# Kernel optimization log

Hardware: AMD Instinct MI355X
Metric: run time of the kernel (lower is better)

The kernel has to match this reference:

```python
import jax, jax.numpy as jnp
import numpy as np
from jax import lax

# MinkowskiEngine semantics reproduced on a dense grid:
# - a sparse tensor's active set = voxels where any feature channel is nonzero
# - stride-1 conv: output coords == input coords  -> mask output with input mask
# - stride-2 conv (k=5, pad=2): output coords = unique(floor(c/2))  -> 2x2x2 max-pool of mask
# - GlobalPooling: mean of features over active output coords, per batch
# MinkowskiConvolution has no bias by default; MinkowskiLinear has one.

DN = ('NCDHW', 'OIDHW', 'NCDHW')

def conv3d(x, w, stride, pad):
    return lax.conv_general_dilated(
        x, w, (stride, stride, stride), [(pad, pad)] * 3, dimension_numbers=DN)

def pool_mask(m):
    # occupancy of stride-2 output coords: any active voxel in each 2x2x2 block
    B, T, H, W = m.shape
    return m.reshape(B, T // 2, 2, H // 2, 2, W // 2, 2).max(axis=(2, 4, 6))

def setup_inputs() -> dict:
    key = jax.random.key(0)
    ks = jax.random.split(key, 7)
    B, T, C, H, W = 16, 128, 2, 34, 34
    vals = jax.random.normal(ks[0], (B, T, C, H, W), jnp.float32)
    keep = jax.random.bernoulli(ks[1], 0.05, (B, T, 1, H, W)).astype(jnp.float32)
    x = vals * keep
    w1 = jax.random.normal(ks[2], (32, 2, 5, 5, 5), jnp.float32) * 0.05
    w2 = jax.random.normal(ks[3], (64, 32, 5, 5, 5), jnp.float32) * 0.05
    w3 = jax.random.normal(ks[4], (128, 64, 3, 3, 3), jnp.float32) * 0.05
    wl = jax.random.normal(ks[5], (10, 128), jnp.float32) * 0.05
    bl = jnp.zeros((10,), jnp.float32)
    return {"x": x, "w1": w1, "w2": w2, "w3": w3, "wl": wl, "bl": bl}

def reference(x, w1, w2, w3, wl, bl):
    # x: [B, T, C, H, W] -> permute(0,2,1,3,4) -> [B, C, T, H, W]
    dense = jnp.transpose(x, (0, 2, 1, 3, 4))
    # active coordinate set of ME.to_sparse(dense)
    mask = (jnp.abs(dense).sum(axis=1) > 0).astype(dense.dtype)  # [B, T, H, W]
    mask = lax.stop_gradient(mask)
    m1 = mask[:, None]
    h = conv3d(dense, w1, 1, 2) * m1                         # k5 s1, out coords = in coords
    mask2 = pool_mask(mask)                                  # stride-2 output occupancy
    m2 = mask2[:, None]
    h = jax.nn.relu(conv3d(h, w2, 2, 2)) * m2                # k5 s2 + ReLU
    h = jax.nn.relu(conv3d(h, w3, 1, 1)) * m2                # k3 s1 + ReLU
    cnt = jnp.maximum(mask2.sum(axis=(1, 2, 3)), 1.0)[:, None]
    pooled = h.sum(axis=(2, 3, 4)) / cnt                     # global avg over active coords -> [B,128]
    logits = pooled @ wl.T + bl                              # MinkowskiLinear(128,10)
    return jax.nn.softmax(jax.nn.relu(logits), axis=-1)      # ReLU -> Softmax -> ToFeature [B,10]
```

## Files before the change

### kernel.cpp

```cpp
#include <hip/hip_runtime.h>

#define BB 16
#define TT 128
#define HH 34
#define WW 34
#define HWSZ (HH*WW)
#define NP1 (BB*TT*HH*WW)
#define TD 64
#define HD 17
#define WD 17
#define NP2 (BB*TD*HD*WD)
#define NW1 (NP1/64)
#define NW2 (NP2/64)
#define CAP1 262144
#define CAP2 131072
#define G2 1024
#define G3 768

typedef __attribute__((ext_vector_type(8))) short bf16x8;
typedef __attribute__((ext_vector_type(4))) float f32x4;

__device__ inline unsigned short f2bf(float f) {
  unsigned u = __float_as_uint(f);
  unsigned r = (u + 0x7fff + ((u >> 16) & 1)) >> 16;
  return (unsigned short)r;
}
__device__ inline float bf2f(unsigned short s) {
  return __uint_as_float((unsigned)s << 16);
}

__global__ void k_ballot1(const float* __restrict__ x, unsigned long long* __restrict__ b1) {
  int i = blockIdx.x * 256 + threadIdx.x;
  int hw = i % HWSZ;
  int bt = i / HWSZ;
  const float* px = x + (size_t)bt * 2 * HWSZ + hw;
  bool act = (fabsf(px[0]) + fabsf(px[HWSZ])) > 0.0f;
  unsigned long long m = __ballot(act);
  if ((threadIdx.x & 63) == 0) b1[i >> 6] = m;
}

__global__ void k_ballot2(const unsigned long long* __restrict__ b1,
                          unsigned long long* __restrict__ b2) {
  int i = blockIdx.x * 256 + threadIdx.x;
  if (i >= NP2) return;
  int ow = i % WD; int r = i / WD;
  int oh = r % HD; r /= HD;
  int od = r % TD; int b = r / TD;
  bool act = false;
  for (int dt = 0; dt < 2; dt++)
    for (int dh = 0; dh < 2; dh++)
      for (int dw = 0; dw < 2; dw++) {
        int t = od * 2 + dt, h = oh * 2 + dh, w = ow * 2 + dw;
        int lin = ((b * TT + t) * HH + h) * WW + w;
        if ((b1[lin >> 6] >> (lin & 63)) & 1ull) act = true;
      }
  unsigned long long m = __ballot(act);
  if ((threadIdx.x & 63) == 0) b2[i >> 6] = m;
}

__global__ __launch_bounds__(1024) void k_scan(
    const unsigned long long* __restrict__ b1, const unsigned long long* __restrict__ b2,
    int* __restrict__ wb1, int* __restrict__ wb2,
    int* __restrict__ counter1, int* __restrict__ counter2, float* __restrict__ cnt) {
  __shared__ int wsum[16];
  __shared__ int wpre[16];
  __shared__ int tots[2];
  int tid = threadIdx.x, lane = tid & 63, wv = tid >> 6;

  const int CH1 = (NW1 + 1023) / 1024;
  int lo = tid * CH1, hi = min(lo + CH1, NW1);
  int s = 0;
  for (int i = lo; i < hi; i++) s += __popcll(b1[i]);
  int sc = s;
  #pragma unroll
  for (int d = 1; d < 64; d <<= 1) { int y = __shfl_up(sc, d); if (lane >= d) sc += y; }
  if (lane == 63) wsum[wv] = sc;
  __syncthreads();
  if (wv == 0 && lane < 16) {
    int v = wsum[lane];
    int p = v;
    #pragma unroll
    for (int d = 1; d < 16; d <<= 1) { int y = __shfl_up(p, d); if (lane >= d) p += y; }
    wpre[lane] = p - v;
    if (lane == 15) tots[0] = p;
  }
  __syncthreads();
  {
    int base = wpre[wv] + (sc - s);
    for (int i = lo; i < hi; i++) { wb1[i] = base; base += __popcll(b1[i]); }
  }
  if (tid == 0) *counter1 = tots[0];
  __syncthreads();

  const int CH2 = (NW2 + 1023) / 1024;
  lo = tid * CH2; hi = min(lo + CH2, NW2);
  s = 0;
  for (int i = lo; i < hi; i++) s += __popcll(b2[i]);
  sc = s;
  #pragma unroll
  for (int d = 1; d < 64; d <<= 1) { int y = __shfl_up(sc, d); if (lane >= d) sc += y; }
  if (lane == 63) wsum[wv] = sc;
  __syncthreads();
  if (wv == 0 && lane < 16) {
    int v = wsum[lane];
    int p = v;
    #pragma unroll
    for (int d = 1; d < 16; d <<= 1) { int y = __shfl_up(p, d); if (lane >= d) p += y; }
    wpre[lane] = p - v;
    if (lane == 15) tots[1] = p;
  }
  __syncthreads();
  {
    int base = wpre[wv] + (sc - s);
    for (int i = lo; i < hi; i++) { wb2[i] = base; base += __popcll(b2[i]); }
  }
  if (tid == 0) *counter2 = tots[1];
  __syncthreads();
  if (tid < 16) {
    int c0 = wb2[tid * 289];
    int c1 = (tid == 15) ? tots[1] : wb2[(tid + 1) * 289];
    cnt[tid] = (float)(c1 - c0);
  }
}

__global__ void k_fill1(const unsigned long long* __restrict__ b1,
                        const int* __restrict__ wb1, int* __restrict__ idx1) {
  int i = blockIdx.x * 256 + threadIdx.x;
  unsigned long long m = b1[i >> 6];
  int lane = i & 63;
  int p = -1;
  if ((m >> lane) & 1ull) {
    p = wb1[i >> 6] + __popcll(m & ((1ull << lane) - 1ull));
    if (p >= CAP1) p = -1;
  }
  idx1[i] = p;
}

__global__ void k_fill2(const unsigned long long* __restrict__ b2,
                        const int* __restrict__ wb2,
                        int* __restrict__ idx2, int* __restrict__ list2) {
  int i = blockIdx.x * 256 + threadIdx.x;
  if (i >= NP2) return;
  unsigned long long m = b2[i >> 6];
  int lane = i & 63;
  int p = -1;
  if ((m >> lane) & 1ull) {
    p = wb2[i >> 6] + __popcll(m & ((1ull << lane) - 1ull));
    if (p < CAP2) list2[p] = i; else p = -1;
  }
  idx2[i] = p;
}

__global__ __launch_bounds__(256) void k_conv1e(
    const float* __restrict__ x, const float* __restrict__ w1,
    const unsigned long long* __restrict__ b1, const int* __restrict__ wb1,
    unsigned short* __restrict__ h1c) {
  __shared__ unsigned short w1s[8000];
  __shared__ unsigned int plist[384];
  __shared__ unsigned long long q[4][128];
  __shared__ int pcnt;
  int tid = threadIdx.x;
  int b = blockIdx.x >> 7;
  int t0 = blockIdx.x & 127;
  if (tid == 0) pcnt = 0;
  for (int j = tid; j < 8000; j += 256) w1s[j] = f2bf(w1[j]);
  __syncthreads();
  int slabbase = (b * TT + t0) * HWSZ;
  for (int hw = tid; hw < HWSZ; hw += 256) {
    int lin = slabbase + hw;
    unsigned long long m = b1[lin >> 6];
    int ln = lin & 63;
    if ((m >> ln) & 1ull) {
      int p = wb1[lin >> 6] + __popcll(m & ((1ull << ln) - 1ull));
      if (p < CAP1) {
        int s = atomicAdd(&pcnt, 1);
        if (s < 384) plist[s] = ((unsigned)p << 11) | (unsigned)hw;
      }
    }
  }
  __syncthreads();
  int n = min(pcnt, 384);
  int lane = tid & 63, wid = tid >> 6;
  int oc = lane & 31, c = lane >> 5;
  int woff = (oc * 2 + c) * 125;
  int csh = c * 16;
  int kt = lane / 5, kh = lane - kt * 5;
  const float* xb = x + (size_t)b * TT * 2 * HWSZ;
  for (int li = wid; li < n; li += 4) {
    unsigned e = plist[li];
    int hw = e & 0x7ff;
    int p = e >> 11;
    int h_ = hw / 34, w_ = hw - h_ * 34;
    int cntA = 0;
    unsigned m5 = 0;
    int t2 = 0, h2 = 0;
    if (lane < 25) {
      t2 = t0 + kt - 2;
      h2 = h_ + kh - 2;
      if ((unsigned)t2 < TT && (unsigned)h2 < HH) {
        int kwmin = (w_ < 2) ? (2 - w_) : 0;
        int kwmax = (w_ > 31) ? (35 - w_) : 4;
        int lin = ((b * TT + t2) * HH + h2) * WW + (w_ + kwmin - 2);
        int wi = lin >> 6, sh = lin & 63;
        unsigned long long v = b1[wi] >> sh;
        if (sh > 59) v |= b1[wi + 1] << (64 - sh);
        m5 = ((unsigned)v & ((1u << (kwmax - kwmin + 1)) - 1u)) << kwmin;
        cntA = __popc(m5);
      }
    }
    int inc = cntA;
    #pragma unroll
    for (int d = 1; d < 64; d <<= 1) { int y = __shfl_up(inc, d); if (lane >= d) inc += y; }
    int off = inc - cntA;
    int ne = __shfl(inc, 63);
    unsigned mm = m5;
    while (mm) {
      int kw = __ffs(mm) - 1; mm &= mm - 1;
      int w2 = w_ + kw - 2;
      int xoff = (t2 * 2) * HWSZ + h2 * 34 + w2;
      unsigned short xv0 = f2bf(xb[xoff]);
      unsigned short xv1 = f2bf(xb[xoff + HWSZ]);
      int tap = (kt * 5 + kh) * 5 + kw;
      q[wid][off++] = (unsigned long long)((unsigned)xv0 | ((unsigned)xv1 << 16)) |
                      ((unsigned long long)tap << 32);
    }
    float acc = 0.f;
    for (int e2 = 0; e2 < ne; e2++) {
      unsigned long long ent = q[wid][e2];
      int tap = (int)(ent >> 32);
      float xv = bf2f((unsigned short)((ent >> csh) & 0xffffull));
      acc += xv * bf2f(w1s[woff + tap]);
    }
    float other = __shfl_down(acc, 32);
    if (lane < 32) h1c[(size_t)p * 32 + oc] = f2bf(acc + other);
  }
}

__global__ void k_tw2b(const float* __restrict__ w2, unsigned short* __restrict__ w2b) {
  int i = blockIdx.x * blockDim.x + threadIdx.x;
  if (i >= 125 * 64 * 32) return;
  int c = i & 31; int r = i >> 5;
  int oc = r & 63; int tap = r >> 6;
  w2b[i] = f2bf(w2[((size_t)oc * 32 + c) * 125 + tap]);
}
__global__ void k_tw3b(const float* __restrict__ w3, unsigned short* __restrict__ w3b) {
  int i = blockIdx.x * blockDim.x + threadIdx.x;
  if (i >= 27 * 128 * 64) return;
  int c = i & 63; int r = i >> 6;
  int oc = r & 127; int tap = r >> 7;
  w3b[i] = f2bf(w3[((size_t)oc * 64 + c) * 27 + tap]);
}

#define S2 40
#define M2 128
__global__ __launch_bounds__(256) void k_conv2m(
    const unsigned short* __restrict__ h1c,
    const unsigned short* __restrict__ w2b,
    const int* __restrict__ idx1,
    const int* __restrict__ list2, const int* __restrict__ counter2,
    unsigned short* __restrict__ h2c) {
  __shared__ __align__(16) unsigned short As[2][M2 * S2];
  __shared__ __align__(16) unsigned short Bs[2][64 * S2];
  __shared__ int4 mc[M2];
  __shared__ int klut[125];
  int tid = threadIdx.x;
  int lane = tid & 63, wid = tid >> 6;
  int fr = lane & 15, fq = lane >> 4;
  int wr = wid * 32;
  if (tid < 125) {
    int kt = tid / 25, r2 = tid - kt * 25;
    klut[tid] = kt | ((r2 / 5) << 4) | ((r2 % 5) << 8);
  }
  int count2 = min(*counter2, CAP2);
  int nchunk = (count2 + M2 - 1) >> 7;
  int aspos = tid >> 1, asq = tid & 1;
  int bspos = tid >> 2, bsq = tid & 3;
  int chid = (blockIdx.x & 7) * (G2 >> 3) + (blockIdx.x >> 3);
  __syncthreads();
  for (int ch = chid; ch < nchunk; ch += gridDim.x) {
    __syncthreads();
    if (tid < M2) {
      int p = ch * M2 + tid;
      int m = (p < count2) ? list2[p] : -1;
      int4 qq; qq.x = -1; qq.y = 0; qq.z = 0; qq.w = 0;
      if (m >= 0) {
        int ow = m % WD; int r = m / WD;
        int oh = r % HD; r /= HD;
        qq.x = r / TD; qq.y = r % TD; qq.z = oh; qq.w = ow;
      }
      mc[tid] = qq;
    }
    __syncthreads();
    int4 q = mc[aspos];
    int tb = q.y * 2 - 2, hb = q.z * 2 - 2, wbv = q.w * 2 - 2;
    bool bok = q.x >= 0;
    auto rowfor = [&](int tap) -> int {
      int k = klut[tap];
      int t = tb + (k & 15), h = hb + ((k >> 4) & 15), w = wbv + (k >> 8);
      int row = -1;
      if (bok && (unsigned)t < TT && (unsigned)h < HH && (unsigned)w < WW)
        row = idx1[((q.x * TT + t) * HH + h) * WW + w];
      return row;
    };
    f32x4 acc[2][4];
    #pragma unroll
    for (int i = 0; i < 2; i++)
      #pragma unroll
      for (int j = 0; j < 4; j++) acc[i][j] = (f32x4){0.f, 0.f, 0.f, 0.f};
    int rowN1;
    int4 rA0 = {0,0,0,0}, rA1 = {0,0,0,0}, rB;
    {
      int r0 = rowfor(0);
      if (r0 >= 0) {
        const unsigned short* s = h1c + (size_t)r0 * 32 + asq * 16;
        rA0 = *(const int4*)s;
        rA1 = *(const int4*)(s + 8);
      }
      rB = *(const int4*)(w2b + (size_t)bspos * 32 + bsq * 8);
      rowN1 = rowfor(1);
    }
    for (int tap = 0; tap < 125; ++tap) {
      int bsel = tap & 1;
      {
        unsigned short* ad = &As[bsel][aspos * S2 + asq * 16];
        *(int4*)(ad) = rA0;
        *(int4*)(ad + 8) = rA1;
        *(int4*)(&Bs[bsel][bspos * S2 + bsq * 8]) = rB;
      }
      bool more = tap < 124;
      if (more) {
        int4 v0 = {0,0,0,0}, v1 = {0,0,0,0};
        if (rowN1 >= 0) {
          const unsigned short* s = h1c + (size_t)rowN1 * 32 + asq * 16;
          v0 = *(const int4*)s;
          v1 = *(const int4*)(s + 8);
        }
        rA0 = v0; rA1 = v1;
        rB = *(const int4*)(w2b + (size_t)(tap + 1) * 2048 + bspos * 32 + bsq * 8);
        rowN1 = (tap < 123) ? rowfor(tap + 2) : -1;
      }
      __syncthreads();
      const unsigned short* ap = &As[bsel][(wr + fr) * S2 + fq * 8];
      const unsigned short* bp = &Bs[bsel][fr * S2 + fq * 8];
      bf16x8 a0 = *(const bf16x8*)ap;
      bf16x8 a1 = *(const bf16x8*)(ap + 16 * S2);
      #pragma unroll
      for (int ni = 0; ni < 4; ni++) {
        bf16x8 bfrag = *(const bf16x8*)(bp + ni * 16 * S2);
        acc[0][ni] = __builtin_amdgcn_mfma_f32_16x16x32_bf16(a0, bfrag, acc[0][ni], 0, 0, 0);
        acc[1][ni] = __builtin_amdgcn_mfma_f32_16x16x32_bf16(a1, bfrag, acc[1][ni], 0, 0, 0);
      }
    }
    int base = ch * M2;
    #pragma unroll
    for (int mi = 0; mi < 2; mi++)
      #pragma unroll
      for (int ni = 0; ni < 4; ni++)
        #pragma unroll
        for (int j = 0; j < 4; j++) {
          int r = wr + mi * 16 + fq * 4 + j;
          int p = base + r;
          if (p < count2) {
            int col = ni * 16 + fr;
            h2c[(size_t)p * 64 + col] = f2bf(fmaxf(acc[mi][ni][j], 0.f));
          }
        }
  }
}

#define S3 72
#define SH3 132
__global__ __launch_bounds__(256) void k_conv3m(
    const unsigned short* __restrict__ h2c,
    const unsigned short* __restrict__ w3b,
    const int* __restrict__ idx2,
    const int* __restrict__ list2, const int* __restrict__ counter2,
    float* __restrict__ partial) {
  __shared__ __align__(16) unsigned short As[2][64 * S3];
  __shared__ __align__(16) unsigned short Bs[2][128 * S3];
  __shared__ float pools[2048];
  __shared__ int rowsL[27 * 64];
  __shared__ int4 mc[64];
  __shared__ int posb[64];
  int tid = threadIdx.x;
  int lane = tid & 63, wid = tid >> 6;
  int fr = lane & 15, fq = lane >> 4;
  int wr = (wid >> 1) * 32, wc = (wid & 1) * 64;
  for (int j = tid; j < 2048; j += 256) pools[j] = 0.f;
  int count2 = min(*counter2, CAP2);
  int nchunk = (count2 + 63) >> 6;
  int spos = tid >> 2, sq = tid & 3;
  int boc = tid >> 1, bh = tid & 1;
  int chid = (blockIdx.x & 7) * (G3 >> 3) + (blockIdx.x >> 3);
  for (int ch = chid; ch < nchunk; ch += gridDim.x) {
    __syncthreads();
    if (tid < 64) {
      int p = ch * 64 + tid;
      int m = (p < count2) ? list2[p] : -1;
      int4 q; q.x = -1; q.y = 0; q.z = 0; q.w = 0;
      if (m >= 0) {
        int ow = m % WD; int r = m / WD;
        int oh = r % HD; r /= HD;
        q.x = r / TD; q.y = r % TD; q.z = oh; q.w = ow;
      }
      mc[tid] = q;
      posb[tid] = (q.x >= 0) ? q.x : 0;
    }
    __syncthreads();
    for (int j = tid; j < 27 * 64; j += 256) {
      int tap = j >> 6, pos = j & 63;
      int4 q = mc[pos];
      int row = -1;
      if (q.x >= 0) {
        int dt = tap / 9 - 1, dh = (tap / 3) % 3 - 1, dw = tap % 3 - 1;
        int t = q.y + dt, h = q.z + dh, w = q.w + dw;
        if ((unsigned)t < TD && (unsigned)h < HD && (unsigned)w < WD)
          row = idx2[((q.x * TD + t) * HD + h) * WD + w];
      }
      rowsL[j] = row;
    }
    __syncthreads();
    f32x4 acc[2][4];
    #pragma unroll
    for (int i = 0; i < 2; i++)
      #pragma unroll
      for (int j = 0; j < 4; j++) acc[i][j] = (f32x4){0.f, 0.f, 0.f, 0.f};
    int4 rA0 = {0, 0, 0, 0}, rA1 = {0, 0, 0, 0};
    {
      int row = rowsL[spos];
      if (row >= 0) {
        const unsigned short* s = h2c + (size_t)row * 64 + sq * 16;
        rA0 = *(const int4*)s;
        rA1 = *(const int4*)(s + 8);
      }
    }
    int4 rB0, rB1, rB2, rB3;
    {
      const unsigned short* wsrc = w3b + (size_t)boc * 64 + bh * 32;
      rB0 = *(const int4*)(wsrc);
      rB1 = *(const int4*)(wsrc + 8);
      rB2 = *(const int4*)(wsrc + 16);
      rB3 = *(const int4*)(wsrc + 24);
    }
    for (int tap = 0; tap < 27; tap++) {
      int bsel = tap & 1;
      {
        unsigned short* ad = &As[bsel][spos * S3 + sq * 16];
        *(int4*)(ad) = rA0;
        *(int4*)(ad + 8) = rA1;
        unsigned short* bd = &Bs[bsel][boc * S3 + bh * 32];
        *(int4*)(bd) = rB0;
        *(int4*)(bd + 8) = rB1;
        *(int4*)(bd + 16) = rB2;
        *(int4*)(bd + 24) = rB3;
      }
      if (tap < 26) {
        int row = rowsL[(tap + 1) * 64 + spos];
        int4 v0 = {0, 0, 0, 0}, v1 = {0, 0, 0, 0};
        if (row >= 0) {
          const unsigned short* s = h2c + (size_t)row * 64 + sq * 16;
          v0 = *(const int4*)s;
          v1 = *(const int4*)(s + 8);
        }
        rA0 = v0; rA1 = v1;
        const unsigned short* wsrc = w3b + ((size_t)(tap + 1) * 128 + boc) * 64 + bh * 32;
        rB0 = *(const int4*)(wsrc);
        rB1 = *(const int4*)(wsrc + 8);
        rB2 = *(const int4*)(wsrc + 16);
        rB3 = *(const int4*)(wsrc + 24);
      }
      __syncthreads();
      const unsigned short* ap = &As[bsel][(wr + fr) * S3 + fq * 8];
      const unsigned short* bp = &Bs[bsel][(wc + fr) * S3 + fq * 8];
      #pragma unroll
      for (int kk = 0; kk < 2; kk++) {
        bf16x8 a0 = *(const bf16x8*)(ap + kk * 32);
        bf16x8 a1 = *(const bf16x8*)(ap + 16 * S3 + kk * 32);
        #pragma unroll
        for (int ni = 0; ni < 4; ni++) {
          bf16x8 bfrag = *(const bf16x8*)(bp + ni * 16 * S3 + kk * 32);
          acc[0][ni] = __builtin_amdgcn_mfma_f32_16x16x32_bf16(a0, bfrag, acc[0][ni], 0, 0, 0);
          acc[1][ni] = __builtin_amdgcn_mfma_f32_16x16x32_bf16(a1, bfrag, acc[1][ni], 0, 0, 0);
        }
      }
    }
    __syncthreads();
    unsigned short* h3 = &As[0][0];
    #pragma unroll
    for (int mi = 0; mi < 2; mi++)
      #pragma unroll
      for (int ni = 0; ni < 4; ni++)
        #pragma unroll
        for (int j = 0; j < 4; j++) {
          int r = wr + mi * 16 + fq * 4 + j;
          int col = wc + ni * 16 + fr;
          h3[r * SH3 + col] = f2bf(fmaxf(acc[mi][ni][j], 0.f));
        }
    __syncthreads();
    if (tid < 128) {
      for (int r = 0; r < 64; r++)
        pools[posb[r] * 128 + tid] += bf2f(h3[r * SH3 + tid]);
    }
  }
  __syncthreads();
  for (int j = tid; j < 2048; j += 256)
    partial[(size_t)blockIdx.x * 2048 + j] = pools[j];
}

__global__ __launch_bounds__(1024) void k_final(
    const float* __restrict__ partial, const float* __restrict__ cnt,
    const float* __restrict__ wl, const float* __restrict__ bl,
    float* __restrict__ out) {
  __shared__ float red[1024];
  __shared__ float pr[128];
  __shared__ float lg[10];
  int b = blockIdx.x;
  int tid = threadIdx.x;
  int c = tid & 127, sl = tid >> 7;
  float s = 0.f;
  for (int g = sl; g < G3; g += 8) s += partial[(size_t)g * 2048 + b * 128 + c];
  red[tid] = s;
  __syncthreads();
  if (tid < 128) {
    float t = 0.f;
    #pragma unroll
    for (int k = 0; k < 8; k++) t += red[k * 128 + tid];
    pr[tid] = t / fmaxf(cnt[b], 1.0f);
  }
  __syncthreads();
  if (tid < 10) {
    float acc = bl[tid];
    for (int j = 0; j < 128; j++) acc += pr[j] * wl[tid * 128 + j];
    lg[tid] = fmaxf(acc, 0.f);
  }
  __syncthreads();
  if (tid == 0) {
    float mx = lg[0];
    for (int k = 1; k < 10; k++) mx = fmaxf(mx, lg[k]);
    float se = 0.f;
    for (int k = 0; k < 10; k++) se += expf(lg[k] - mx);
    for (int k = 0; k < 10; k++) out[b * 10 + k] = expf(lg[k] - mx) / se;
  }
}

extern "C" void kernel_launch(void* const* d_in, const int* in_sizes, int n_in,
                              void* d_out, int out_size, void* d_ws, size_t ws_size,
                              hipStream_t stream) {
  const float* x  = (const float*)d_in[0];
  const float* w1 = (const float*)d_in[1];
  const float* w2 = (const float*)d_in[2];
  const float* w3 = (const float*)d_in[3];
  const float* wl = (const float*)d_in[4];
  const float* bl = (const float*)d_in[5];
  float* out = (float*)d_out;

  float* ws = (float*)d_ws;
  int* counter1 = (int*)(ws + 0);
  int* counter2 = (int*)(ws + 1);
  float* cnt = ws + 16;
  size_t off = 2080;
  unsigned long long* b1 = (unsigned long long*)(ws + off); off += NW1 * 2 + 2;
  unsigned long long* b2 = (unsigned long long*)(ws + off); off += NW2 * 2;
  int* wb1 = (int*)(ws + off); off += NW1;
  int* wb2 = (int*)(ws + off); off += NW2;
  int* idx1 = (int*)(ws + off); off += NP1;
  unsigned short* h1c = (unsigned short*)(ws + off); off += (size_t)CAP1 * 16;
  int* idx2 = (int*)(ws + off); off += NP2;
  int* list2 = (int*)(ws + off); off += CAP2;
  unsigned short* h2c = (unsigned short*)(ws + off); off += (size_t)CAP2 * 32;
  unsigned short* w2b = (unsigned short*)(ws + off); off += 128000;
  unsigned short* w3b = (unsigned short*)(ws + off); off += 110592;
  float* partial = ws + off; off += (size_t)G3 * 2048;

  hipMemsetAsync(d_ws, 0, 256, stream);

  k_tw2b<<<(256000 + 255) / 256, 256, 0, stream>>>(w2, w2b);
  k_tw3b<<<(221184 + 255) / 256, 256, 0, stream>>>(w3, w3b);
  k_ballot1<<<NP1 / 256, 256, 0, stream>>>(x, b1);
  k_ballot2<<<(NP2 + 255) / 256, 256, 0, stream>>>(b1, b2);
  k_scan<<<1, 1024, 0, stream>>>(b1, b2, wb1, wb2, counter1, counter2, cnt);
  k_conv1e<<<2048, 256, 0, stream>>>(x, w1, b1, wb1, h1c);
  k_fill1<<<NP1 / 256, 256, 0, stream>>>(b1, wb1, idx1);
  k_fill2<<<(NP2 + 255) / 256, 256, 0, stream>>>(b2, wb2, idx2, list2);
  k_conv2m<<<G2, 256, 0, stream>>>(h1c, w2b, idx1, list2, counter2, h2c);
  k_conv3m<<<G3, 256, 0, stream>>>(h2c, w3b, idx2, list2, counter2, partial);
  k_final<<<16, 1024, 0, stream>>>(partial, cnt, wl, bl, out);
}
```

Baseline: 413.4 us.

## Replace dense index maps with on-the-fly bitmap popcount lookups; split final reduction

Removes the dense idx1/idx2 index arrays and their fill kernels. conv2 and conv3 now compute a voxel's compact row from the occupancy bitmap word and the per-word prefix base with a popcount, which cuts a full-grid write pass and shrinks the gathered data. The final reduction is split into a wider 128-block reduce kernel plus a small head kernel, the conv3 grid shrinks, and LDS row strides are changed. The trade-off is extra ALU work and two dependent loads per neighbour lookup, and the new LDS padding may introduce bank conflicts.

Measured after the change: 1.039 ms. 151% more time.

```diff
diff --git a/kernel.cpp b/kernel.cpp
--- a/kernel.cpp
+++ b/kernel.cpp
@@ -15,7 +15,7 @@
 #define CAP1 262144
 #define CAP2 131072
 #define G2 1024
-#define G3 768
+#define G3 512
 
 typedef __attribute__((ext_vector_type(8))) short bf16x8;
 typedef __attribute__((ext_vector_type(4))) float f32x4;
@@ -123,32 +123,16 @@
   }
 }
 
-__global__ void k_fill1(const unsigned long long* __restrict__ b1,
-                        const int* __restrict__ wb1, int* __restrict__ idx1) {
-  int i = blockIdx.x * 256 + threadIdx.x;
-  unsigned long long m = b1[i >> 6];
-  int lane = i & 63;
-  int p = -1;
-  if ((m >> lane) & 1ull) {
-    p = wb1[i >> 6] + __popcll(m & ((1ull << lane) - 1ull));
-    if (p >= CAP1) p = -1;
-  }
-  idx1[i] = p;
-}
-
-__global__ void k_fill2(const unsigned long long* __restrict__ b2,
-                        const int* __restrict__ wb2,
-                        int* __restrict__ idx2, int* __restrict__ list2) {
+__global__ void k_list2(const unsigned long long* __restrict__ b2,
+                        const int* __restrict__ wb2, int* __restrict__ list2) {
   int i = blockIdx.x * 256 + threadIdx.x;
   if (i >= NP2) return;
   unsigned long long m = b2[i >> 6];
   int lane = i & 63;
-  int p = -1;
   if ((m >> lane) & 1ull) {
-    p = wb2[i >> 6] + __popcll(m & ((1ull << lane) - 1ull));
-    if (p < CAP2) list2[p] = i; else p = -1;
-  }
-  idx2[i] = p;
+    int p = wb2[i >> 6] + __popcll(m & ((1ull << lane) - 1ull));
+    if (p < CAP2) list2[p] = i;
+  }
 }
 
 __global__ __launch_bounds__(256) void k_conv1e(
@@ -251,12 +235,12 @@
   w3b[i] = f2bf(w3[((size_t)oc * 64 + c) * 27 + tap]);
 }
 
-#define S2 40
+#define S2 36
 #define M2 128
 __global__ __launch_bounds__(256) void k_conv2m(
     const unsigned short* __restrict__ h1c,
     const unsigned short* __restrict__ w2b,
-    const int* __restrict__ idx1,
+    const unsigned long long* __restrict__ b1, const int* __restrict__ wb1,
     const int* __restrict__ list2, const int* __restrict__ counter2,
     unsigned short* __restrict__ h2c) {
   __shared__ __align__(16) unsigned short As[2][M2 * S2];
@@ -298,8 +282,15 @@
       int k = klut[tap];
       int t = tb + (k & 15), h = hb + ((k >> 4) & 15), w = wbv + (k >> 8);
       int row = -1;
-      if (bok && (unsigned)t < TT && (unsigned)h < HH && (unsigned)w < WW)
-        row = idx1[((q.x * TT + t) * HH + h) * WW + w];
+      if (bok && (unsigned)t < TT && (unsigned)h < HH && (unsigned)w < WW) {
+        int lin = ((q.x * TT + t) * HH + h) * WW + w;
+        unsigned long long m = b1[lin >> 6];
+        int ln = lin & 63;
+        if ((m >> ln) & 1ull) {
+          row = wb1[lin >> 6] + __popcll(m & ((1ull << ln) - 1ull));
+          if (row >= CAP1) row = -1;
+        }
+      }
       return row;
     };
     f32x4 acc[2][4];
@@ -368,12 +359,12 @@
   }
 }
 
-#define S3 72
+#define S3 68
 #define SH3 132
 __global__ __launch_bounds__(256) void k_conv3m(
     const unsigned short* __restrict__ h2c,
     const unsigned short* __restrict__ w3b,
-    const int* __restrict__ idx2,
+    const unsigned long long* __restrict__ b2, const int* __restrict__ wb2,
     const int* __restrict__ list2, const int* __restrict__ counter2,
     float* __restrict__ partial) {
   __shared__ __align__(16) unsigned short As[2][64 * S3];
@@ -414,8 +405,15 @@
       if (q.x >= 0) {
         int dt = tap / 9 - 1, dh = (tap / 3) % 3 - 1, dw = tap % 3 - 1;
         int t = q.y + dt, h = q.z + dh, w = q.w + dw;
-        if ((unsigned)t < TD && (unsigned)h < HD && (unsigned)w < WD)
-          row = idx2[((q.x * TD + t) * HD + h) * WD + w];
+        if ((unsigned)t < TD && (unsigned)h < HD && (unsigned)w < WD) {
+          int lin = ((q.x * TD + t) * HD + h) * WD + w;
+          unsigned long long m = b2[lin >> 6];
+          int ln = lin & 63;
+          if ((m >> ln) & 1ull) {
+            row = wb2[lin >> 6] + __popcll(m & ((1ull << ln) - 1ull));
+            if (row >= CAP2) row = -1;
+          }
+        }
       }
       rowsL[j] = row;
     }
@@ -507,26 +505,31 @@
     partial[(size_t)blockIdx.x * 2048 + j] = pools[j];
 }
 
-__global__ __launch_bounds__(1024) void k_final(
-    const float* __restrict__ partial, const float* __restrict__ cnt,
-    const float* __restrict__ wl, const float* __restrict__ bl,
-    float* __restrict__ out) {
-  __shared__ float red[1024];
+__global__ __launch_bounds__(256) void k_red(
+    const float* __restrict__ partial, float* __restrict__ pooled) {
+  __shared__ float red[256];
+  int o = blockIdx.x * 16 + (threadIdx.x & 15);
+  int sl = threadIdx.x >> 4;
+  float s = 0.f;
+  for (int g = sl; g < G3; g += 16) s += partial[(size_t)g * 2048 + o];
+  red[threadIdx.x] = s;
+  __syncthreads();
+  if (threadIdx.x < 16) {
+    float t = 0.f;
+    #pragma unroll
+    for (int k = 0; k < 16; k++) t += red[k * 16 + threadIdx.x];
+    pooled[o] = t;
+  }
+}
+
+__global__ void k_fin(const float* __restrict__ pooled, const float* __restrict__ cnt,
+                      const float* __restrict__ wl, const float* __restrict__ bl,
+                      float* __restrict__ out) {
   __shared__ float pr[128];
   __shared__ float lg[10];
   int b = blockIdx.x;
   int tid = threadIdx.x;
-  int c = tid & 127, sl = tid >> 7;
-  float s = 0.f;
-  for (int g = sl; g < G3; g += 8) s += partial[(size_t)g * 2048 + b * 128 + c];
-  red[tid] = s;
-  __syncthreads();
-  if (tid < 128) {
-    float t = 0.f;
-    #pragma unroll
-    for (int k = 0; k < 8; k++) t += red[k * 128 + tid];
-    pr[tid] = t / fmaxf(cnt[b], 1.0f);
-  }
+  pr[tid] = pooled[b * 128 + tid] / fmaxf(cnt[b], 1.0f);
   __syncthreads();
   if (tid < 10) {
     float acc = bl[tid];
@@ -558,14 +561,13 @@
   int* counter1 = (int*)(ws + 0);
   int* counter2 = (int*)(ws + 1);
   float* cnt = ws + 16;
+  float* pooled = ws + 32;
   size_t off = 2080;
   unsigned long long* b1 = (unsigned long long*)(ws + off); off += NW1 * 2 + 2;
   unsigned long long* b2 = (unsigned long long*)(ws + off); off += NW2 * 2;
   int* wb1 = (int*)(ws + off); off += NW1;
   int* wb2 = (int*)(ws + off); off += NW2;
-  int* idx1 = (int*)(ws + off); off += NP1;
   unsigned short* h1c = (unsigned short*)(ws + off); off += (size_t)CAP1 * 16;
-  int* idx2 = (int*)(ws + off); off += NP2;
   int* list2 = (int*)(ws + off); off += CAP2;
   unsigned short* h2c = (unsigned short*)(ws + off); off += (size_t)CAP2 * 32;
   unsigned short* w2b = (unsigned short*)(ws + off); off += 128000;
@@ -580,9 +582,9 @@
   k_ballot2<<<(NP2 + 255) / 256, 256, 0, stream>>>(b1, b2);
   k_scan<<<1, 1024, 0, stream>>>(b1, b2, wb1, wb2, counter1, counter2, cnt);
   k_conv1e<<<2048, 256, 0, stream>>>(x, w1, b1, wb1, h1c);
-  k_fill1<<<NP1 / 256, 256, 0, stream>>>(b1, wb1, idx1);
-  k_fill2<<<(NP2 + 255) / 256, 256, 0, stream>>>(b2, wb2, idx2, list2);
-  k_conv2m<<<G2, 256, 0, stream>>>(h1c, w2b, idx1, list2, counter2, h2c);
-  k_conv3m<<<G3, 256, 0, stream>>>(h2c, w3b, idx2, list2, counter2, partial);
-  k_final<<<16, 1024, 0, stream>>>(partial, cnt, wl, bl, out);
-}
+  k_list2<<<(NP2 + 255) / 256, 256, 0, stream>>>(b2, wb2, list2);
+  k_conv2m<<<G2, 256, 0, stream>>>(h1c, w2b, b1, wb1, list2, counter2, h2c);
+  k_conv3m<<<G3, 256, 0, stream>>>(h2c, w3b, b2, wb2, list2, counter2, partial);
+  k_red<<<128, 256, 0, stream>>>(partial, pooled);
+  k_fin<<<16, 128, 0, stream>>>(pooled, cnt, wl, bl, out);
+}
```
